# Kernel optimization log

Hardware: AMD Instinct MI355X
Metric: run time of the kernel (lower is better)

Reference implementation:

```python
import jax, jax.numpy as jnp
import numpy as np
from jax import lax

T, C_IN, H0, W0 = 15, 6, 160, 160
C1, C2 = 128, 256
K1, K2 = 5, 2
THR1, THR2 = 10.0, 1.0
KWTA, RAD = 8, 1
W_MEAN, W_STD = 0.8, 0.05


def setup_inputs() -> dict:
    key = jax.random.key(0)
    k1, k2, k3 = jax.random.split(key, 3)
    # cumulative binary spike wave: each input neuron fires at a random time (or never)
    t_fire = jax.random.randint(k1, (C_IN, H0, W0), 0, 2 * T)
    inp = (jnp.arange(T)[:, None, None, None] >= t_fire[None]).astype(jnp.float32)
    w1 = W_MEAN + W_STD * jax.random.normal(k2, (C1, C_IN, K1, K1), jnp.float32)
    w2 = W_MEAN + W_STD * jax.random.normal(k3, (C2, C1, K2, K2), jnp.float32)
    return {"inp": inp, "w1": w1, "w2": w2, "layer_idx": 2}


def _conv(x, w):
    # x: [T, C, H, W] (time acts as batch), VALID conv, no bias (SpykeTorch snn.Convolution)
    return lax.conv_general_dilated(x, w, (1, 1), 'VALID',
                                    dimension_numbers=('NCHW', 'OIHW', 'NCHW'))


def _pad(x, p):
    return jnp.pad(x, ((0, 0), (0, 0), (p, p), (p, p)))


def _pool(x):
    # sf.pooling(s, 2, 2, 1): max-pool kernel 2, stride 2, padding 1 per time step
    return lax.reduce_window(x, -jnp.inf, lax.max,
                             (1, 1, 2, 2), (1, 1, 2, 2),
                             ((0, 0), (0, 0), (1, 1), (1, 1)))


def _fire(v, thr):
    # sf.fire with return_thresholded_potentials=True: zero out sub-threshold potentials
    v = jnp.where(v < thr, 0.0, v)
    return jnp.sign(v), v


def _pointwise_inhibition(v):
    # v: [T, C, H, W] nonneg.  At each spatial position, the feature with the max
    t, c = v.shape[0], v.shape[1]
    max_vals = v.max(axis=1)                      # [T,H,W]
    max_idx = v.argmax(axis=1).astype(jnp.int32)  # [T,H,W] winner channel per time
    clamp = jnp.sign(max_vals)                    # [T,H,W] any-spike indicator
    earliest = jnp.clip(t - clamp.sum(axis=0).astype(jnp.int32), 0, t - 1)  # [H,W]
    winner = jnp.take_along_axis(max_idx, earliest[None], axis=0)[0]        # [H,W]
    alive = clamp[-1]                             # [H,W] 1 if any spike ever
    coef = (jnp.arange(c)[:, None, None] == winner[None]).astype(v.dtype) * alive
    return v * coef[None]


def _get_k_winners(v, s, kwta, rad):
    # Greedy k-WTA with per-feature and spatial (radius) inhibition (NMS-like).
    t, c, h, w = v.shape
    earliest = jnp.clip(t - s.sum(axis=0).astype(jnp.int32), 0, t - 1)  # [C,H,W]
    vals = jnp.take_along_axis(v, earliest[None], axis=0)[0]            # potential at first spike
    trunc = s * vals
    big = trunc.max() * t                                               # earlier-spike dominance term
    trunc = trunc + s * big
    total = trunc.sum(axis=0)                                           # [C,H,W]

    ch_ids = jnp.arange(c)
    row_ids = jnp.arange(h)
    col_ids = jnp.arange(w)

    def step(total, _):
        idx = jnp.argmax(total.reshape(-1))
        mv = total.reshape(-1)[idx]
        f = (idx // (h * w)).astype(jnp.int32)
        rem = idx % (h * w)
        r = (rem // w).astype(jnp.int32)
        col = (rem % w).astype(jnp.int32)
        active = mv != 0
        kill = ((ch_ids == f)[:, None, None]
                | ((jnp.abs(row_ids - r) <= rad)[:, None]
                   & (jnp.abs(col_ids - col) <= rad)[None, :])[None])
        new_total = jnp.where(active, jnp.where(kill, 0.0, total), total)
        winner = jnp.where(active, jnp.stack([f, r, col]), -1)
        return new_total, winner

    _, winners = lax.scan(step, total, None, length=kwta)
    return winners  # [kwta, 3] (feature,row,col), -1 rows = inactive


def reference(inp, w1, w2, layer_idx):
    # training path, layer_idx == 2 (deepest branch)
    x = _pad(inp, 2)                       # [T,6,164,164]
    v = _conv(x, w1)                       # [T,128,160,160]
    s, v = _fire(v, THR1)
    s_in = _pad(_pool(s), 1)               # [T,128,83,83]
    s_in = _pointwise_inhibition(s_in)
    v = _conv(s_in, w2)                    # [T,256,82,82]
    s, v = _fire(v, THR2)
    v = _pointwise_inhibition(v)
    s = jnp.sign(v)
    winners = _get_k_winners(v, s, KWTA, RAD)
    return s, v, winners
```

## Files before the change

### kernel.cpp

```cpp
#include <hip/hip_runtime.h>

#define T_ 15
#define CIN 6
#define H0 160
#define W0 160
#define C1_ 128
#define C2_ 256
#define HP 83
#define H2 82
#define NPIX (H0*W0)
#define NIN (CIN*NPIX)
#define NPOS (H2*H2)
#define NS (T_*C2_*NPOS)
#define THR1 10.0f
#define THR2 1.0f

__global__ __launch_bounds__(256) void k0_tf(const float* __restrict__ inp,
                                             const float* __restrict__ w1,
                                             unsigned char* __restrict__ tf,
                                             float* __restrict__ wT) {
    int b = blockIdx.x;
    if (b < NIN / 256) {
        int i = b * 256 + threadIdx.x;
        float c = 0.f;
#pragma unroll
        for (int t = 0; t < T_; t++) c += inp[(size_t)t * NIN + i];
        tf[i] = (unsigned char)(15 - (int)(c + 0.5f));
    } else {
        int idx = (b - NIN / 256) * 256 + threadIdx.x;
        if (idx < 150 * C1_) {
            int j = idx >> 7, c = idx & 127;
            wT[idx] = w1[c * 150 + j];
        }
    }
}

__global__ __launch_bounds__(256) void k0b_sort(const unsigned char* __restrict__ tfin,
                                                unsigned char* __restrict__ perm,
                                                unsigned char* __restrict__ cumb) {
    __shared__ int cnt[16 * 256];
    int tid = threadIdx.x;
    int ty0 = (blockIdx.x / 10) * 16, tx0 = (blockIdx.x % 10) * 16;
    int tyl = tid >> 4, txl = tid & 15;
    int y = ty0 + tyl, x = tx0 + txl;
    int pix = y * W0 + x;

    unsigned int pk[19];
#pragma unroll
    for (int u = 0; u < 19; u++) pk[u] = 0u;
#pragma unroll
    for (int j = 0; j < 150; j++) {
        int ci = j / 25, r = j % 25, ky = r / 5, kx = r % 5;
        int yy = y + ky - 2, xx = x + kx - 2;
        unsigned int tfv = ((unsigned)yy < (unsigned)H0 && (unsigned)xx < (unsigned)W0)
                               ? (unsigned)tfin[ci * NPIX + yy * W0 + xx] : 15u;
        pk[j >> 3] |= tfv << ((j & 7) * 4);
    }

    int* col = cnt + tid;
#pragma unroll
    for (int t = 0; t < 16; t++) col[t * 256] = 0;
#pragma unroll
    for (int j = 0; j < 150; j++) {
        unsigned int tfv = (pk[j >> 3] >> ((j & 7) * 4)) & 15u;
        col[tfv * 256]++;
    }

    int c[15];
#pragma unroll
    for (int t = 0; t < 15; t++) c[t] = col[t * 256];

    unsigned int w0 = 0, wA = 0, wB = 0, wC = 0;
    int acc = 0;
#pragma unroll
    for (int t = 0; t < 15; t++) {
        acc += c[t];
        if (t < 4)       w0 |= (unsigned)acc << (8 * t);
        else if (t < 8)  wA |= (unsigned)acc << (8 * (t - 4));
        else if (t < 12) wB |= (unsigned)acc << (8 * (t - 8));
        else             wC |= (unsigned)acc << (8 * (t - 12));
    }
    *(uint4*)(cumb + (size_t)pix * 16) = make_uint4(w0, wA, wB, wC);

    int s = 0;
#pragma unroll
    for (int t = 0; t < 15; t++) { col[t * 256] = s; s += c[t]; }

    unsigned char* pr = perm + (size_t)pix * 160;
#pragma unroll
    for (int j = 0; j < 150; j++) {
        unsigned int tfv = (pk[j >> 3] >> ((j & 7) * 4)) & 15u;
        if (tfv < 15u) { int pos = col[tfv * 256]++; pr[pos] = (unsigned char)j; }
    }
}

__global__ __launch_bounds__(256) void k1_main(const unsigned char* __restrict__ perm,
                                               const unsigned char* __restrict__ cumb,
                                               const float* __restrict__ wT,
                                               unsigned char* __restrict__ fst1) {
    int wid = blockIdx.x * 4 + (threadIdx.x >> 6);
    int lane = threadIdx.x & 63;
    for (int pix = wid; pix < NPIX; pix += 6400) {
        uint4 cw = *(const uint4*)(cumb + (size_t)pix * 16);
        const unsigned char* pp = perm + (size_t)pix * 160;
        const float* wb = wT + 2 * lane;
        float v0 = 0.f, v1 = 0.f;
        int f0 = 15, f1 = 15, i = 0;

#define K1STEP(TT, CE)                                                          \
        {                                                                       \
            int ce = __builtin_amdgcn_readfirstlane((int)(CE));                 \
            float b0 = 0.f, b1 = 0.f;                                           \
            for (; i < ce; ++i) {                                               \
                int j = pp[i];                                                  \
                float2 w = *(const float2*)(wb + j * C1_);                      \
                b0 += w.x; b1 += w.y;                                           \
            }                                                                   \
            v0 += b0; v1 += b1;                                                 \
            if (f0 == 15 && v0 >= THR1) f0 = TT;                                \
            if (f1 == 15 && v1 >= THR1) f1 = TT;                                \
            if (__all((f0 < 15) & (f1 < 15))) goto done;                        \
        }

        K1STEP(0,  cw.x & 255u)         K1STEP(1,  (cw.x >> 8) & 255u)
        K1STEP(2,  (cw.x >> 16) & 255u) K1STEP(3,  (cw.x >> 24) & 255u)
        K1STEP(4,  cw.y & 255u)         K1STEP(5,  (cw.y >> 8) & 255u)
        K1STEP(6,  (cw.y >> 16) & 255u) K1STEP(7,  (cw.y >> 24) & 255u)
        K1STEP(8,  cw.z & 255u)         K1STEP(9,  (cw.z >> 8) & 255u)
        K1STEP(10, (cw.z >> 16) & 255u) K1STEP(11, (cw.z >> 24) & 255u)
        K1STEP(12, cw.w & 255u)         K1STEP(13, (cw.w >> 8) & 255u)
        K1STEP(14, (cw.w >> 16) & 255u)
#undef K1STEP
done:
        *(uchar2*)(fst1 + (size_t)pix * C1_ + 2 * lane) =
            make_uchar2((unsigned char)f0, (unsigned char)f1);
    }
}

__global__ __launch_bounds__(256) void k2_pool(const unsigned char* __restrict__ fst1,
                                               unsigned char* __restrict__ win_t,
                                               unsigned char* __restrict__ win_ch) {
    int pos = blockIdx.x * 4 + (threadIdx.x >> 6);
    int lane = threadIdx.x & 63;
    if (pos >= HP * HP) return;
    int py = pos / HP, px = pos % HP;
    if (py == 0 || py == HP - 1 || px == 0 || px == HP - 1) {
        if (lane == 0) { win_t[pos] = 15; win_ch[pos] = 0; }
        return;
    }
    int y0 = 2 * py - 3, x0 = 2 * px - 3;
    int m0 = 15, m1 = 15;
#pragma unroll
    for (int dy = 0; dy < 2; dy++) {
        int y = y0 + dy;
        if ((unsigned)y < (unsigned)H0) {
#pragma unroll
            for (int dx = 0; dx < 2; dx++) {
                int x = x0 + dx;
                if ((unsigned)x < (unsigned)W0) {
                    uchar2 f = *(const uchar2*)(fst1 + (size_t)(y * W0 + x) * C1_ + 2 * lane);
                    m0 = f.x < m0 ? f.x : m0;
                    m1 = f.y < m1 ? f.y : m1;
                }
            }
        }
    }
    int k0 = (m0 << 8) | (2 * lane);
    int k1 = (m1 << 8) | (2 * lane + 1);
    int key = k0 < k1 ? k0 : k1;
#pragma unroll
    for (int off = 32; off > 0; off >>= 1) {
        int other = __shfl_xor(key, off);
        key = other < key ? other : key;
    }
    if (lane == 0) {
        win_t[pos] = (unsigned char)(key >> 8);
        win_ch[pos] = (unsigned char)(key & 255);
    }
}

__global__ __launch_bounds__(256) void kz_fill(uint4* __restrict__ dst, size_t n16,
                                               unsigned int* __restrict__ bigbits) {
    size_t stride = (size_t)gridDim.x * 256;
    uint4 z = make_uint4(0u, 0u, 0u, 0u);
    for (size_t i = (size_t)blockIdx.x * 256 + threadIdx.x; i < n16; i += stride)
        dst[i] = z;
    if (blockIdx.x == 0 && threadIdx.x == 0) *bigbits = 0u;
}

__global__ __launch_bounds__(256) void k3_conv2(const unsigned char* __restrict__ win_t,
                                                const unsigned char* __restrict__ win_ch,
                                                const float* __restrict__ w2,
                                                float* __restrict__ s_out,
                                                float* __restrict__ v_out,
                                                float* __restrict__ vals,
                                                int* __restrict__ nsp_arr,
                                                int* __restrict__ ow_arr,
                                                unsigned int* __restrict__ bigbits) {
    __shared__ unsigned int ormask;
    __shared__ unsigned long long amax;
    int p = blockIdx.x;
    int y2 = p / H2, x2 = p % H2;
    int o = threadIdx.x;
    if (o == 0) { ormask = 0u; amax = 0ull; }
    __syncthreads();

    float w[4]; int tj[4];
#pragma unroll
    for (int k = 0; k < 4; k++) {
        int dy = k >> 1, dx = k & 1;
        int pi = (y2 + dy) * HP + (x2 + dx);
        int tt = win_t[pi];
        int cc = win_ch[pi];
        tj[k] = tt;
        w[k] = (tt < 15) ? w2[(o * C1_ + cc) * 4 + k] : 0.0f;
    }

    float z[T_];
    unsigned int m = 0u;
#pragma unroll
    for (int t = 0; t < T_; t++) {
        float v = 0.f;
#pragma unroll
        for (int k = 0; k < 4; k++) v += (t >= tj[k]) ? w[k] : 0.f;
        float zz = (v < THR2) ? 0.f : v;
        z[t] = zz;
        m |= (zz > 0.f) ? (1u << t) : 0u;
    }

    unsigned int mw = m;
#pragma unroll
    for (int off = 32; off > 0; off >>= 1) mw |= __shfl_xor(mw, off);
    if ((o & 63) == 0) atomicOr(&ormask, mw);
    __syncthreads();

    unsigned int om = ormask;
    int count = __popc(om & 0x7FFFu);
    int earliest = 15 - count;
    earliest = earliest < 0 ? 0 : (earliest > 14 ? 14 : earliest);
    int alive = (om >> 14) & 1;

    float zval = 0.f;
#pragma unroll
    for (int t = 0; t < T_; t++) zval = (t == earliest) ? z[t] : zval;

    unsigned long long key =
        ((unsigned long long)__float_as_uint(zval) << 16) | (unsigned long long)(1023 - o);
#pragma unroll
    for (int off = 32; off > 0; off >>= 1) {
        unsigned long long other = __shfl_xor(key, off);
        key = other > key ? other : key;
    }
    if ((o & 63) == 0) atomicMax(&amax, key);
    __syncthreads();

    if (alive) {
        int wo = 1023 - (int)(amax & 0xFFFFull);
        if (o == wo) {
            int nsp = __popc(m & 0x7FFFu);
            int e2 = 15 - nsp;
            e2 = e2 < 0 ? 0 : (e2 > 14 ? 14 : e2);
            float vv = 0.f;
#pragma unroll
            for (int t = 0; t < T_; t++) vv = (t == e2) ? z[t] : vv;
            vals[p] = vv; nsp_arr[p] = nsp; ow_arr[p] = wo;
            if (nsp > 0) atomicMax(bigbits, __float_as_uint(vv));
#pragma unroll
            for (int t = 0; t < T_; t++) {
                if (z[t] != 0.f) {
                    int idx = ((t * C2_ + wo) * H2 + y2) * H2 + x2;
                    v_out[idx] = z[t];
                    s_out[idx] = 1.0f;
                }
            }
        }
    } else if (o == 0) {
        vals[p] = 0.f; nsp_arr[p] = 0; ow_arr[p] = 0;
    }
}

__global__ __launch_bounds__(1024) void k4_kwta(const float* __restrict__ vals,
                                                const int* __restrict__ nsp,
                                                const int* __restrict__ ow,
                                                const unsigned int* __restrict__ bigbits,
                                                float* __restrict__ wout) {
    __shared__ float tot[NPOS];
    __shared__ short och[NPOS];
    __shared__ unsigned long long amax;
    int tid = threadIdx.x;
    float big = __uint_as_float(*bigbits) * 15.0f;

    for (int p = tid; p < NPOS; p += 1024) {
        int n = nsp[p];
        tot[p] = (n > 0) ? (float)n * (vals[p] + big) : 0.0f;
        och[p] = (short)ow[p];
    }
    if (tid == 0) amax = 0ull;
    __syncthreads();

    for (int it = 0; it < 8; it++) {
        unsigned long long best = 0ull;
        for (int p = tid; p < NPOS; p += 1024) {
            float tv = tot[p];
            if (tv > 0.0f) {
                unsigned int k = (unsigned)och[p] * (unsigned)NPOS + (unsigned)p;
                unsigned long long pk =
                    ((unsigned long long)__float_as_uint(tv) << 21) |
                    (unsigned long long)(0x1FFFFFu - k);
                best = pk > best ? pk : best;
            }
        }
#pragma unroll
        for (int off = 32; off > 0; off >>= 1) {
            unsigned long long other = __shfl_xor(best, off);
            best = other > best ? other : best;
        }
        if ((tid & 63) == 0) atomicMax(&amax, best);
        __syncthreads();
        unsigned long long mx = amax;
        __syncthreads();
        if (tid == 0) amax = 0ull;

        if (mx == 0ull) {
            if (tid == 0) {
                wout[it * 3 + 0] = -1.f; wout[it * 3 + 1] = -1.f; wout[it * 3 + 2] = -1.f;
            }
        } else {
            unsigned int k = 0x1FFFFFu - (unsigned)(mx & 0x1FFFFFull);
            int f = (int)(k / NPOS), pp = (int)(k % NPOS);
            int r = pp / H2, col = pp % H2;
            if (tid == 0) {
                wout[it * 3 + 0] = (float)f; wout[it * 3 + 1] = (float)r; wout[it * 3 + 2] = (float)col;
            }
            for (int p = tid; p < NPOS; p += 1024) {
                int pr = p / H2, pc = p % H2;
                bool kill = (och[p] == (short)f) ||
                            (pr >= r - 1 && pr <= r + 1 && pc >= col - 1 && pc <= col + 1);
                if (kill) tot[p] = 0.0f;
            }
        }
        __syncthreads();
    }
}

extern "C" void kernel_launch(void* const* d_in, const int* in_sizes, int n_in,
                              void* d_out, int out_size, void* d_ws, size_t ws_size,
                              hipStream_t stream) {
    const float* inp = (const float*)d_in[0];
    const float* w1  = (const float*)d_in[1];
    const float* w2  = (const float*)d_in[2];

    float* out = (float*)d_out;
    float* s_out = out;
    float* v_out = out + (size_t)NS;
    float* wnr   = out + 2 * (size_t)NS;

    char* scratch = (char*)d_out + (size_t)NS * sizeof(float);
    unsigned char* tfin = (unsigned char*)scratch;
    float*         wT   = (float*)(scratch + (256 << 10));
    unsigned char* cumb = (unsigned char*)(scratch + (512 << 10));
    unsigned char* perm = (unsigned char*)(scratch + (1 << 20));
    unsigned char* fst1 = (unsigned char*)(scratch + (5 << 20));

    unsigned char* win_t  = (unsigned char*)d_ws;
    unsigned char* win_ch = (unsigned char*)d_ws + 8192;
    float* vals = (float*)((char*)d_ws + 16384);
    int*   nsp  = (int*)((char*)d_ws + 49152);
    int*   ow   = (int*)((char*)d_ws + 81920);
    unsigned int* bigbits = (unsigned int*)((char*)d_ws + 114688);

    hipLaunchKernelGGL(k0_tf, dim3(NIN / 256 + 75), dim3(256), 0, stream, inp, w1, tfin, wT);
    hipLaunchKernelGGL(k0b_sort, dim3(100), dim3(256), 0, stream, tfin, perm, cumb);
    hipLaunchKernelGGL(k1_main, dim3(1600), dim3(256), 0, stream, perm, cumb, wT, fst1);
    hipLaunchKernelGGL(k2_pool, dim3((HP * HP + 3) / 4), dim3(256), 0, stream,
                       fst1, win_t, win_ch);

    size_t n16 = (size_t)out_size / 4;
    hipLaunchKernelGGL(kz_fill, dim3(4096), dim3(256), 0, stream,
                       (uint4*)d_out, n16, bigbits);

    hipLaunchKernelGGL(k3_conv2, dim3(NPOS), dim3(256), 0, stream,
                       win_t, win_ch, w2, s_out, v_out, vals, nsp, ow, bigbits);
    hipLaunchKernelGGL(k4_kwta, dim3(1), dim3(1024), 0, stream, vals, nsp, ow, bigbits, wnr);
}
```

Baseline: 218.8 us.

## Fuse preprocessing into mega kernel, use per-time bitmasks, single-wave kWTA

Merges the first-spike-time computation, the sort kernel, the weight transposes and the output zero-fill into one multi-role launch. Instead of a sorted permutation list with cumulative counts, it now stores per-time 32-bit masks of which kernel taps fire, and conv1 iterates set bits with ctz. It also adds a transposed w2 for coalesced loads in conv2 and rewrites kWTA as a single 64-lane wave with precomputed 64-bit keys and no block barriers on atomics. The aim is fewer launches and better overlap of the fill with compute. The cost is scratch moved into the workspace when it is large enough, with a fallback path otherwise, and more mask reads per pixel in conv1.

After: 347.6 us. 1.59x slower.

```diff
diff --git a/kernel.cpp b/kernel.cpp
--- a/kernel.cpp
+++ b/kernel.cpp
@@ -15,123 +15,102 @@
 #define THR1 10.0f
 #define THR2 1.0f
 
-__global__ __launch_bounds__(256) void k0_tf(const float* __restrict__ inp,
-                                             const float* __restrict__ w1,
-                                             unsigned char* __restrict__ tf,
-                                             float* __restrict__ wT) {
+__global__ __launch_bounds__(256) void k_mega(const float* __restrict__ inp,
+                                              const float* __restrict__ w1,
+                                              const float* __restrict__ w2,
+                                              unsigned int* __restrict__ maskg,
+                                              float* __restrict__ w1T,
+                                              float* __restrict__ w2T,
+                                              unsigned int* __restrict__ bigbits,
+                                              uint4* __restrict__ fill_dst,
+                                              size_t n16, int nfill) {
+    __shared__ unsigned char tft[CIN * 20 * 20];
+    __shared__ int cnt[16 * 256];
     int b = blockIdx.x;
-    if (b < NIN / 256) {
-        int i = b * 256 + threadIdx.x;
-        float c = 0.f;
-#pragma unroll
-        for (int t = 0; t < T_; t++) c += inp[(size_t)t * NIN + i];
-        tf[i] = (unsigned char)(15 - (int)(c + 0.5f));
+    int tid = threadIdx.x;
+
+    if (b < 100) {
+        int ty0 = (b / 10) * 16, tx0 = (b % 10) * 16;
+        for (int i = tid; i < CIN * 400; i += 256) {
+            int ci = i / 400, rem = i % 400;
+            int ly = rem / 20, lx = rem % 20;
+            int y = ty0 + ly - 2, x = tx0 + lx - 2;
+            unsigned char tv = 15;
+            if ((unsigned)y < (unsigned)H0 && (unsigned)x < (unsigned)W0) {
+                float c = 0.f;
+                int base = ci * NPIX + y * W0 + x;
+#pragma unroll
+                for (int t = 0; t < T_; t++) c += inp[(size_t)t * NIN + base];
+                tv = (unsigned char)(15 - (int)(c + 0.5f));
+            }
+            tft[i] = tv;
+        }
+        __syncthreads();
+
+        int tyl = tid >> 4, txl = tid & 15;
+        int pix = (ty0 + tyl) * W0 + (tx0 + txl);
+        int* col = cnt + tid;
+
+#pragma unroll
+        for (int w = 0; w < 5; w++) {
+            int j0 = w * 32, j1 = (w == 4) ? 150 : (j0 + 32);
+#pragma unroll
+            for (int q = 0; q < 16; q++) col[q * 256] = 0;
+#pragma unroll 32
+            for (int j = j0; j < j1; j++) {
+                int ci = j / 25, r = j % 25, ky = r / 5, kx = r % 5;
+                int tfv = tft[ci * 400 + (tyl + ky) * 20 + (txl + kx)];
+                col[tfv * 256] |= 1u << (j & 31);
+            }
+#pragma unroll
+            for (int t = 0; t < 15; t++)
+                maskg[(size_t)(t * 5 + w) * NPIX + pix] = (unsigned)col[t * 256];
+        }
+    } else if (b < 175) {
+        if (b == 100 && tid == 0) *bigbits = 0u;
+        int idx = (b - 100) * 256 + tid;
+        int j = idx >> 7, c = idx & 127;
+        w1T[idx] = w1[c * 150 + j];
+    } else if (b < 687) {
+        int idx = (b - 175) * 256 + tid;
+        int o = idx & 255, kcc = idx >> 8;
+        int cc = kcc & 127, k = kcc >> 7;
+        w2T[idx] = w2[o * 512 + cc * 4 + k];
     } else {
-        int idx = (b - NIN / 256) * 256 + threadIdx.x;
-        if (idx < 150 * C1_) {
-            int j = idx >> 7, c = idx & 127;
-            wT[idx] = w1[c * 150 + j];
-        }
-    }
-}
-
-__global__ __launch_bounds__(256) void k0b_sort(const unsigned char* __restrict__ tfin,
-                                                unsigned char* __restrict__ perm,
-                                                unsigned char* __restrict__ cumb) {
-    __shared__ int cnt[16 * 256];
-    int tid = threadIdx.x;
-    int ty0 = (blockIdx.x / 10) * 16, tx0 = (blockIdx.x % 10) * 16;
-    int tyl = tid >> 4, txl = tid & 15;
-    int y = ty0 + tyl, x = tx0 + txl;
-    int pix = y * W0 + x;
-
-    unsigned int pk[19];
-#pragma unroll
-    for (int u = 0; u < 19; u++) pk[u] = 0u;
-#pragma unroll
-    for (int j = 0; j < 150; j++) {
-        int ci = j / 25, r = j % 25, ky = r / 5, kx = r % 5;
-        int yy = y + ky - 2, xx = x + kx - 2;
-        unsigned int tfv = ((unsigned)yy < (unsigned)H0 && (unsigned)xx < (unsigned)W0)
-                               ? (unsigned)tfin[ci * NPIX + yy * W0 + xx] : 15u;
-        pk[j >> 3] |= tfv << ((j & 7) * 4);
-    }
-
-    int* col = cnt + tid;
-#pragma unroll
-    for (int t = 0; t < 16; t++) col[t * 256] = 0;
-#pragma unroll
-    for (int j = 0; j < 150; j++) {
-        unsigned int tfv = (pk[j >> 3] >> ((j & 7) * 4)) & 15u;
-        col[tfv * 256]++;
-    }
-
-    int c[15];
-#pragma unroll
-    for (int t = 0; t < 15; t++) c[t] = col[t * 256];
-
-    unsigned int w0 = 0, wA = 0, wB = 0, wC = 0;
-    int acc = 0;
-#pragma unroll
-    for (int t = 0; t < 15; t++) {
-        acc += c[t];
-        if (t < 4)       w0 |= (unsigned)acc << (8 * t);
-        else if (t < 8)  wA |= (unsigned)acc << (8 * (t - 4));
-        else if (t < 12) wB |= (unsigned)acc << (8 * (t - 8));
-        else             wC |= (unsigned)acc << (8 * (t - 12));
-    }
-    *(uint4*)(cumb + (size_t)pix * 16) = make_uint4(w0, wA, wB, wC);
-
-    int s = 0;
-#pragma unroll
-    for (int t = 0; t < 15; t++) { col[t * 256] = s; s += c[t]; }
-
-    unsigned char* pr = perm + (size_t)pix * 160;
-#pragma unroll
-    for (int j = 0; j < 150; j++) {
-        unsigned int tfv = (pk[j >> 3] >> ((j & 7) * 4)) & 15u;
-        if (tfv < 15u) { int pos = col[tfv * 256]++; pr[pos] = (unsigned char)j; }
-    }
-}
-
-__global__ __launch_bounds__(256) void k1_main(const unsigned char* __restrict__ perm,
-                                               const unsigned char* __restrict__ cumb,
-                                               const float* __restrict__ wT,
+        size_t stride = (size_t)nfill * 256;
+        uint4 z = make_uint4(0u, 0u, 0u, 0u);
+        for (size_t i = (size_t)(b - 687) * 256 + tid; i < n16; i += stride)
+            fill_dst[i] = z;
+    }
+}
+
+__global__ __launch_bounds__(256) void k1_main(const unsigned int* __restrict__ maskg,
+                                               const float* __restrict__ w1T,
                                                unsigned char* __restrict__ fst1) {
     int wid = blockIdx.x * 4 + (threadIdx.x >> 6);
     int lane = threadIdx.x & 63;
+    const float* wb = w1T + 2 * lane;
     for (int pix = wid; pix < NPIX; pix += 6400) {
-        uint4 cw = *(const uint4*)(cumb + (size_t)pix * 16);
-        const unsigned char* pp = perm + (size_t)pix * 160;
-        const float* wb = wT + 2 * lane;
         float v0 = 0.f, v1 = 0.f;
-        int f0 = 15, f1 = 15, i = 0;
-
-#define K1STEP(TT, CE)                                                          \
-        {                                                                       \
-            int ce = __builtin_amdgcn_readfirstlane((int)(CE));                 \
-            float b0 = 0.f, b1 = 0.f;                                           \
-            for (; i < ce; ++i) {                                               \
-                int j = pp[i];                                                  \
-                float2 w = *(const float2*)(wb + j * C1_);                      \
-                b0 += w.x; b1 += w.y;                                           \
-            }                                                                   \
-            v0 += b0; v1 += b1;                                                 \
-            if (f0 == 15 && v0 >= THR1) f0 = TT;                                \
-            if (f1 == 15 && v1 >= THR1) f1 = TT;                                \
-            if (__all((f0 < 15) & (f1 < 15))) goto done;                        \
-        }
-
-        K1STEP(0,  cw.x & 255u)         K1STEP(1,  (cw.x >> 8) & 255u)
-        K1STEP(2,  (cw.x >> 16) & 255u) K1STEP(3,  (cw.x >> 24) & 255u)
-        K1STEP(4,  cw.y & 255u)         K1STEP(5,  (cw.y >> 8) & 255u)
-        K1STEP(6,  (cw.y >> 16) & 255u) K1STEP(7,  (cw.y >> 24) & 255u)
-        K1STEP(8,  cw.z & 255u)         K1STEP(9,  (cw.z >> 8) & 255u)
-        K1STEP(10, (cw.z >> 16) & 255u) K1STEP(11, (cw.z >> 24) & 255u)
-        K1STEP(12, cw.w & 255u)         K1STEP(13, (cw.w >> 8) & 255u)
-        K1STEP(14, (cw.w >> 16) & 255u)
-#undef K1STEP
-done:
+        int f0 = 15, f1 = 15;
+        for (int t = 0; t < 15; ++t) {
+            float b0 = 0.f, b1 = 0.f;
+#pragma unroll
+            for (int w = 0; w < 5; ++w) {
+                unsigned int m = maskg[(size_t)(t * 5 + w) * NPIX + pix];
+                int base = w * 32;
+                while (m) {
+                    int j = base + __builtin_ctz(m);
+                    m &= m - 1;
+                    float2 ww = *(const float2*)(wb + j * C1_);
+                    b0 += ww.x; b1 += ww.y;
+                }
+            }
+            v0 += b0; v1 += b1;
+            f0 = (f0 == 15 && v0 >= THR1) ? t : f0;
+            f1 = (f1 == 15 && v1 >= THR1) ? t : f1;
+            if (__all((f0 < 15) & (f1 < 15))) break;
+        }
         *(uchar2*)(fst1 + (size_t)pix * C1_ + 2 * lane) =
             make_uchar2((unsigned char)f0, (unsigned char)f1);
     }
@@ -190,7 +169,7 @@
 
 __global__ __launch_bounds__(256) void k3_conv2(const unsigned char* __restrict__ win_t,
                                                 const unsigned char* __restrict__ win_ch,
-                                                const float* __restrict__ w2,
+                                                const float* __restrict__ w2T,
                                                 float* __restrict__ s_out,
                                                 float* __restrict__ v_out,
                                                 float* __restrict__ vals,
@@ -213,7 +192,7 @@
         int tt = win_t[pi];
         int cc = win_ch[pi];
         tj[k] = tt;
-        w[k] = (tt < 15) ? w2[(o * C1_ + cc) * 4 + k] : 0.0f;
+        w[k] = (tt < 15) ? w2T[(k * C1_ + cc) * 256 + o] : 0.0f;
     }
 
     float z[T_];
@@ -279,65 +258,58 @@
     }
 }
 
-__global__ __launch_bounds__(1024) void k4_kwta(const float* __restrict__ vals,
-                                                const int* __restrict__ nsp,
-                                                const int* __restrict__ ow,
-                                                const unsigned int* __restrict__ bigbits,
-                                                float* __restrict__ wout) {
-    __shared__ float tot[NPOS];
-    __shared__ short och[NPOS];
-    __shared__ unsigned long long amax;
-    int tid = threadIdx.x;
+__global__ __launch_bounds__(64) void k4_kwta(const float* __restrict__ vals,
+                                              const int* __restrict__ nsp,
+                                              const int* __restrict__ ow,
+                                              const unsigned int* __restrict__ bigbits,
+                                              float* __restrict__ wout) {
+    __shared__ unsigned long long keyl[NPOS];
+    __shared__ unsigned char och[NPOS];
+    int lane = threadIdx.x;
     float big = __uint_as_float(*bigbits) * 15.0f;
 
-    for (int p = tid; p < NPOS; p += 1024) {
+    for (int p = lane; p < NPOS; p += 64) {
         int n = nsp[p];
-        tot[p] = (n > 0) ? (float)n * (vals[p] + big) : 0.0f;
-        och[p] = (short)ow[p];
-    }
-    if (tid == 0) amax = 0ull;
+        int f = ow[p];
+        float tv = (n > 0) ? (float)n * (vals[p] + big) : 0.0f;
+        unsigned int k = (unsigned)f * (unsigned)NPOS + (unsigned)p;
+        keyl[p] = (tv > 0.0f)
+                      ? (((unsigned long long)__float_as_uint(tv) << 21) |
+                         (unsigned long long)(0x1FFFFFu - k))
+                      : 0ull;
+        och[p] = (unsigned char)f;
+    }
     __syncthreads();
 
     for (int it = 0; it < 8; it++) {
         unsigned long long best = 0ull;
-        for (int p = tid; p < NPOS; p += 1024) {
-            float tv = tot[p];
-            if (tv > 0.0f) {
-                unsigned int k = (unsigned)och[p] * (unsigned)NPOS + (unsigned)p;
-                unsigned long long pk =
-                    ((unsigned long long)__float_as_uint(tv) << 21) |
-                    (unsigned long long)(0x1FFFFFu - k);
-                best = pk > best ? pk : best;
-            }
+        for (int p = lane; p < NPOS; p += 64) {
+            unsigned long long kk = keyl[p];
+            best = kk > best ? kk : best;
         }
 #pragma unroll
         for (int off = 32; off > 0; off >>= 1) {
             unsigned long long other = __shfl_xor(best, off);
             best = other > best ? other : best;
         }
-        if ((tid & 63) == 0) atomicMax(&amax, best);
-        __syncthreads();
-        unsigned long long mx = amax;
-        __syncthreads();
-        if (tid == 0) amax = 0ull;
-
-        if (mx == 0ull) {
-            if (tid == 0) {
+        if (best == 0ull) {
+            if (lane == 0) {
                 wout[it * 3 + 0] = -1.f; wout[it * 3 + 1] = -1.f; wout[it * 3 + 2] = -1.f;
             }
-        } else {
-            unsigned int k = 0x1FFFFFu - (unsigned)(mx & 0x1FFFFFull);
-            int f = (int)(k / NPOS), pp = (int)(k % NPOS);
-            int r = pp / H2, col = pp % H2;
-            if (tid == 0) {
-                wout[it * 3 + 0] = (float)f; wout[it * 3 + 1] = (float)r; wout[it * 3 + 2] = (float)col;
-            }
-            for (int p = tid; p < NPOS; p += 1024) {
-                int pr = p / H2, pc = p % H2;
-                bool kill = (och[p] == (short)f) ||
-                            (pr >= r - 1 && pr <= r + 1 && pc >= col - 1 && pc <= col + 1);
-                if (kill) tot[p] = 0.0f;
-            }
+            __syncthreads();
+            continue;
+        }
+        unsigned int k = 0x1FFFFFu - (unsigned)(best & 0x1FFFFFull);
+        int f = (int)(k / NPOS), pp = (int)(k % NPOS);
+        int r = pp / H2, col = pp % H2;
+        if (lane == 0) {
+            wout[it * 3 + 0] = (float)f; wout[it * 3 + 1] = (float)r; wout[it * 3 + 2] = (float)col;
+        }
+        for (int p = lane; p < NPOS; p += 64) {
+            int pr = p / H2, pc = p % H2;
+            bool kill = (och[p] == (unsigned char)f) ||
+                        (pr >= r - 1 && pr <= r + 1 && pc >= col - 1 && pc <= col + 1);
+            if (kill) keyl[p] = 0ull;
         }
         __syncthreads();
     }
@@ -355,31 +327,34 @@
     float* v_out = out + (size_t)NS;
     float* wnr   = out + 2 * (size_t)NS;
 
-    char* scratch = (char*)d_out + (size_t)NS * sizeof(float);
-    unsigned char* tfin = (unsigned char*)scratch;
-    float*         wT   = (float*)(scratch + (256 << 10));
-    unsigned char* cumb = (unsigned char*)(scratch + (512 << 10));
-    unsigned char* perm = (unsigned char*)(scratch + (1 << 20));
-    unsigned char* fst1 = (unsigned char*)(scratch + (5 << 20));
-
-    unsigned char* win_t  = (unsigned char*)d_ws;
-    unsigned char* win_ch = (unsigned char*)d_ws + 8192;
-    float* vals = (float*)((char*)d_ws + 16384);
-    int*   nsp  = (int*)((char*)d_ws + 49152);
-    int*   ow   = (int*)((char*)d_ws + 81920);
-    unsigned int* bigbits = (unsigned int*)((char*)d_ws + 114688);
-
-    hipLaunchKernelGGL(k0_tf, dim3(NIN / 256 + 75), dim3(256), 0, stream, inp, w1, tfin, wT);
-    hipLaunchKernelGGL(k0b_sort, dim3(100), dim3(256), 0, stream, tfin, perm, cumb);
-    hipLaunchKernelGGL(k1_main, dim3(1600), dim3(256), 0, stream, perm, cumb, wT, fst1);
+    size_t need = (size_t)15 << 20;
+    bool big_ws = ws_size >= need;
+    char* scratch = big_ws ? (char*)d_ws
+                           : (char*)d_out + (size_t)NS * sizeof(float);
+    unsigned int* maskg = (unsigned int*)scratch;
+    unsigned char* fst1 = (unsigned char*)(scratch + (8 << 20));
+    float* w1T = (float*)(scratch + (12 << 20));
+    float* w2T = (float*)(scratch + (13 << 20));
+    char* smol = big_ws ? (char*)d_ws + (14 << 20) : (char*)d_ws;
+    unsigned char* win_t  = (unsigned char*)smol;
+    unsigned char* win_ch = (unsigned char*)smol + 8192;
+    float* vals = (float*)(smol + 16384);
+    int*   nsp  = (int*)(smol + 49152);
+    int*   ow   = (int*)(smol + 81920);
+    unsigned int* bigbits = (unsigned int*)(smol + 114688);
+
+    size_t n16 = (size_t)out_size / 4;
+    int nfill = big_ws ? 4096 : 0;
+
+    hipLaunchKernelGGL(k_mega, dim3(687 + nfill), dim3(256), 0, stream,
+                       inp, w1, w2, maskg, w1T, w2T, bigbits, (uint4*)d_out, n16, nfill);
+    hipLaunchKernelGGL(k1_main, dim3(1600), dim3(256), 0, stream, maskg, w1T, fst1);
     hipLaunchKernelGGL(k2_pool, dim3((HP * HP + 3) / 4), dim3(256), 0, stream,
                        fst1, win_t, win_ch);
-
-    size_t n16 = (size_t)out_size / 4;
-    hipLaunchKernelGGL(kz_fill, dim3(4096), dim3(256), 0, stream,
-                       (uint4*)d_out, n16, bigbits);
-
+    if (!big_ws)
+        hipLaunchKernelGGL(kz_fill, dim3(4096), dim3(256), 0, stream,
+                           (uint4*)d_out, n16, bigbits);
     hipLaunchKernelGGL(k3_conv2, dim3(NPOS), dim3(256), 0, stream,
-                       win_t, win_ch, w2, s_out, v_out, vals, nsp, ow, bigbits);
-    hipLaunchKernelGGL(k4_kwta, dim3(1), dim3(1024), 0, stream, vals, nsp, ow, bigbits, wnr);
-}
+                       win_t, win_ch, w2T, s_out, v_out, vals, nsp, ow, bigbits);
+    hipLaunchKernelGGL(k4_kwta, dim3(1), dim3(64), 0, stream, vals, nsp, ow, bigbits, wnr);
+}
```
